# Kernel optimization log

Measured on AMD Instinct MI355X. Metric: run time of the kernel, lower is better.

Reference implementation:

```python
import jax, jax.numpy as jnp
import numpy as np


def _dequantize_and_unpack(packed, scales):
    """packed: [d_out, d_in//2] int8, each byte holds two 4-bit nibbles.
    Returns [d_out, d_in] in scales.dtype, scaled per output row."""
    low = (packed & 15).astype(jnp.int8)
    high = (packed >> 4).astype(jnp.int8)  # arithmetic shift, like torch int8 >> 4
    low = jnp.where(low > 7, low - 16, low)
    high = jnp.where(high > 7, high - 16, high)
    # interleave: even cols = high nibble, odd cols = low nibble
    w = jnp.stack([high, low], axis=-1).reshape(packed.shape[0], -1)
    return w.astype(scales.dtype) * scales


def setup_inputs() -> dict:
    key = jax.random.key(0)
    ks = jax.random.split(key, 7)
    d = 4096
    N = 4096
    x = jax.random.normal(ks[0], (N, d), dtype=jnp.float32)
    fc1_weights_packed = jax.random.randint(ks[1], (2 * d, d // 2), -8, 7, dtype=jnp.int32).astype(jnp.int8)
    fc1_scales = (jax.random.normal(ks[2], (2 * d, 1), dtype=jnp.float32) * 0.02).astype(jnp.float16)
    fc1_bias = jax.random.normal(ks[3], (2 * d,), dtype=jnp.float32)
    fc2_weights_packed = jax.random.randint(ks[4], (d, d), -8, 7, dtype=jnp.int32).astype(jnp.int8)
    fc2_scales = (jax.random.normal(ks[5], (d, 1), dtype=jnp.float32) * 0.02).astype(jnp.float16)
    fc2_bias = jax.random.normal(ks[6], (d,), dtype=jnp.float32)
    return {
        "x": x,
        "fc1_weights_packed": fc1_weights_packed,
        "fc1_scales": fc1_scales,
        "fc1_bias": fc1_bias,
        "fc2_weights_packed": fc2_weights_packed,
        "fc2_scales": fc2_scales,
        "fc2_bias": fc2_bias,
    }


def reference(x, fc1_weights_packed, fc1_scales, fc1_bias,
              fc2_weights_packed, fc2_scales, fc2_bias):
    # fc1: dequantize to [2d, d], linear, relu
    w1 = _dequantize_and_unpack(fc1_weights_packed, fc1_scales).astype(x.dtype)
    h = jax.nn.relu(jnp.dot(x, w1.T) + fc1_bias)
    # fc2: dequantize to [d, 2d], linear
    w2 = _dequantize_and_unpack(fc2_weights_packed, fc2_scales).astype(x.dtype)
    return jnp.dot(h, w2.T) + fc2_bias
```

## Files before the change

kernel.cpp:

```cpp
#include <hip/hip_runtime.h>
#include <hip/hip_fp16.h>
#include <stdint.h>


typedef __attribute__((ext_vector_type(4)))  int i32x4;
typedef __attribute__((ext_vector_type(16))) int i32x16;
typedef __attribute__((ext_vector_type(8))) _Float16 f16x8;

__device__ __forceinline__ void load_lds16(const void* g, void* l) {
    __builtin_amdgcn_global_load_lds(
        (__attribute__((address_space(1))) void*)(void*)g,
        (__attribute__((address_space(3))) void*)(void*)l,
        16, 0, 0);
}

__device__ __forceinline__ float block_max(float m, int tid) {
    __shared__ float red[4];
#pragma unroll
    for (int off = 32; off; off >>= 1)
        m = fmaxf(m, __shfl_down(m, off, 64));
    if ((tid & 63) == 0) red[tid >> 6] = m;
    __syncthreads();
    m = fmaxf(fmaxf(red[0], red[1]), fmaxf(red[2], red[3]));
    __syncthreads();
    return m;
}

__global__ __launch_bounds__(256) void quant_x(
    const float* __restrict__ in, int* __restrict__ out,
    float* __restrict__ rscale, int ncols)
{
    const int tid = threadIdx.x;
    const int row = blockIdx.x;
    const float4* rp = (const float4*)(in + (size_t)row * ncols);
    const int nf4 = ncols / 4;
    float4 v[4];
    float m = 0.f;
#pragma unroll
    for (int k = 0; k < 4; ++k) {
        v[k] = rp[k * 256 + tid];
        m = fmaxf(m, fmaxf(fmaxf(fabsf(v[k].x), fabsf(v[k].y)),
                           fmaxf(fabsf(v[k].z), fabsf(v[k].w))));
    }
    m = block_max(m, tid);
    m = fmaxf(m, 1e-20f);
    const float inv = 127.f / m;
    if (tid == 0) rscale[row] = m / 127.f;
    int* orow = out + (size_t)row * nf4;
#pragma unroll
    for (int k = 0; k < 4; ++k) {
        int q0 = __float2int_rn(v[k].x * inv);
        int q1 = __float2int_rn(v[k].y * inv);
        int q2 = __float2int_rn(v[k].z * inv);
        int q3 = __float2int_rn(v[k].w * inv);
        orow[k * 256 + tid] = (q0 & 0xFF) | ((q1 & 0xFF) << 8) |
                              ((q2 & 0xFF) << 16) | ((q3 & 0xFF) << 24);
    }
}

__global__ __launch_bounds__(256) void quant_h(
    const _Float16* __restrict__ in, int2* __restrict__ out,
    float* __restrict__ rscale, int ncols)
{
    const int tid = threadIdx.x;
    const int row = blockIdx.x;
    const f16x8* rp = (const f16x8*)(in + (size_t)row * ncols);
    const int nv = ncols / 8;
    f16x8 v[4];
    float m = 0.f;
#pragma unroll
    for (int k = 0; k < 4; ++k) {
        v[k] = rp[k * 256 + tid];
#pragma unroll
        for (int e = 0; e < 8; ++e) m = fmaxf(m, (float)v[k][e]);
    }
    m = block_max(m, tid);
    m = fmaxf(m, 1e-20f);
    const float inv = 255.f / m;
    if (tid == 0) rscale[row] = m / 255.f;
    int2* orow = out + (size_t)row * nv;
#pragma unroll
    for (int k = 0; k < 4; ++k) {
        union { int8_t b[8]; int2 w; } u;
#pragma unroll
        for (int e = 0; e < 8; ++e) {
            int q = __float2int_rn((float)v[k][e] * inv);
            q = q < 0 ? 0 : (q > 255 ? 255 : q);
            u.b[e] = (int8_t)(q - 128);
        }
        orow[k * 256 + tid] = u.w;
    }
}

__global__ __launch_bounds__(256) void expand_int4_i8(
    const int4* __restrict__ packed, int2* __restrict__ out,
    int* __restrict__ wsum, int n_i4)
{
    const int tid = threadIdx.x;
    const int row = blockIdx.x;
    const int4* prow = packed + (size_t)row * n_i4;
    int2* orow = out + (size_t)row * n_i4;
    int sum = 0;
    for (int j = tid; j < n_i4; j += 256) {
        int4 p = prow[j];
        int vals[4] = {p.x, p.y, p.z, p.w};
        union { int8_t b[8]; int2 w; } u;
#pragma unroll
        for (int b = 0; b < 4; ++b) {
            int by = (int)(int8_t)(vals[b] & 0xFF);
            int hi = by >> 4;
            int lo = ((by & 15) ^ 8) - 8;
            u.b[2 * b] = (int8_t)hi;
            u.b[2 * b + 1] = (int8_t)lo;
            sum += hi + lo;
        }
        orow[j] = u.w;
    }
    __shared__ int sred[4];
#pragma unroll
    for (int off = 32; off; off >>= 1) sum += __shfl_down(sum, off, 64);
    if ((tid & 63) == 0) sred[tid >> 6] = sum;
    __syncthreads();
    if (tid == 0) wsum[row] = sred[0] + sred[1] + sred[2] + sred[3];
}

template <bool RELU, bool SHIFT, typename OutT>
__global__ __launch_bounds__(512, 2) void gemm_i8_256(
    const int8_t* __restrict__ A, const int8_t* __restrict__ B,
    OutT* __restrict__ C,
    const float* __restrict__ sa,
    const float* __restrict__ s,
    const float* __restrict__ bias,
    const int* __restrict__ wsum,
    int M, int N, int K)
{
    __shared__ alignas(16) char sA[2][256 * 128];
    __shared__ alignas(16) char sB[2][256 * 128];

    const int tid  = threadIdx.x;
    const int lane = tid & 63;
    const int wave = tid >> 6;
    const int wm = wave >> 2;
    const int wn = wave & 3;

    const int nwg = gridDim.x * gridDim.y;
    int bid = blockIdx.y * gridDim.x + blockIdx.x;
    const int cpx = nwg >> 3;
    bid = (bid & 7) * cpx + (bid >> 3);
    const int bm = (bid / gridDim.x) * 256;
    const int bn = (bid % gridDim.x) * 256;

    const int srow = tid >> 3;
    const int scol = ((tid & 7) ^ (srow & 7)) << 4;
    const int8_t* Ag = A + (size_t)(bm + srow) * K + scol;
    const int8_t* Bg = B + (size_t)(bn + srow) * K + scol;
    const size_t rK64 = (size_t)64 * K;
    const int ldst = tid * 16;

    auto stage_a = [&](int buf, int h, int kt) {
        const int8_t* g = Ag + (size_t)h * 128 * K + (size_t)kt * 128;
        char* l = &sA[buf][h * 16384 + ldst];
        load_lds16(g, l);
        load_lds16(g + rK64, l + 8192);
    };
    auto stage_b = [&](int buf, int h, int kt) {
        const int8_t* g = Bg + (size_t)h * 128 * K + (size_t)kt * 128;
        char* l = &sB[buf][h * 16384 + ldst];
        load_lds16(g, l);
        load_lds16(g + rK64, l + 8192);
    };

    const int l31 = lane & 31;
    const int kh  = lane >> 5;
    int coff[4];
#pragma unroll
    for (int ks = 0; ks < 4; ++ks)
        coff[ks] = (((ks * 2 + kh) ^ (l31 & 7)) << 4);
    int abase[4], bbase[2];
#pragma unroll
    for (int i = 0; i < 4; ++i) abase[i] = (wm * 128 + i * 32 + l31) * 128;
#pragma unroll
    for (int j = 0; j < 2; ++j) bbase[j] = (wn * 64 + j * 32 + l31) * 128;

    i32x16 acc[4][2] = {};
    const int NT = K >> 7;

    stage_a(0, 0, 0); stage_a(0, 1, 0);
    stage_b(0, 0, 0); stage_b(0, 1, 0);
    if (NT > 1) { stage_b(1, 0, 1); stage_b(1, 1, 1); }

    for (int t = 0; t < NT; ++t) {
        const char* pA = sA[t & 1];
        const char* pB = sB[t & 1];
        if (t + 1 < NT) asm volatile("s_waitcnt vmcnt(4)" ::: "memory");
        else            asm volatile("s_waitcnt vmcnt(0)" ::: "memory");
        __builtin_amdgcn_s_barrier();
        __builtin_amdgcn_sched_barrier(0);

        i32x4 bf[2][4];
        {
            i32x4 af[4];
#pragma unroll
            for (int j = 0; j < 2; ++j)
#pragma unroll
                for (int ks = 0; ks < 4; ++ks)
                    bf[j][ks] = *(const i32x4*)(pB + bbase[j] + coff[ks]);
#pragma unroll
            for (int ks = 0; ks < 4; ++ks)
                af[ks] = *(const i32x4*)(pA + abase[0] + coff[ks]);
            if (t + 1 < NT) stage_a((t + 1) & 1, 0, t + 1);
            __builtin_amdgcn_s_barrier();
            asm volatile("s_waitcnt lgkmcnt(0)" ::: "memory");
            __builtin_amdgcn_sched_barrier(0);
            __builtin_amdgcn_s_setprio(1);
#pragma unroll
            for (int ks = 0; ks < 4; ++ks) {
                acc[0][0] = __builtin_amdgcn_mfma_i32_32x32x32_i8(
                    af[ks], bf[0][ks], acc[0][0], 0, 0, 0);
                acc[0][1] = __builtin_amdgcn_mfma_i32_32x32x32_i8(
                    af[ks], bf[1][ks], acc[0][1], 0, 0, 0);
            }
            __builtin_amdgcn_s_setprio(0);
            __builtin_amdgcn_s_barrier();
        }
#pragma unroll
        for (int i = 1; i < 4; ++i) {
            i32x4 af[4];
#pragma unroll
            for (int ks = 0; ks < 4; ++ks)
                af[ks] = *(const i32x4*)(pA + abase[i] + coff[ks]);
            if (i == 1)      { if (t + 1 < NT) stage_a((t + 1) & 1, 1, t + 1); }
            else if (i == 2) { if (t + 2 < NT) stage_b(t & 1, 0, t + 2); }
            else             { if (t + 2 < NT) stage_b(t & 1, 1, t + 2); }
            __builtin_amdgcn_s_barrier();
            asm volatile("s_waitcnt lgkmcnt(0)" ::: "memory");
            __builtin_amdgcn_sched_barrier(0);
            __builtin_amdgcn_s_setprio(1);
#pragma unroll
            for (int ks = 0; ks < 4; ++ks) {
                acc[i][0] = __builtin_amdgcn_mfma_i32_32x32x32_i8(
                    af[ks], bf[0][ks], acc[i][0], 0, 0, 0);
                acc[i][1] = __builtin_amdgcn_mfma_i32_32x32x32_i8(
                    af[ks], bf[1][ks], acc[i][1], 0, 0, 0);
            }
            __builtin_amdgcn_s_setprio(0);
            __builtin_amdgcn_s_barrier();
        }
    }

#pragma unroll
    for (int j = 0; j < 2; ++j) {
        const int n  = bn + wn * 64 + j * 32 + l31;
        const float sc = s[n];
        const float bs = bias[n];
        const int shf = SHIFT ? 128 * wsum[n] : 0;
#pragma unroll
        for (int i = 0; i < 4; ++i) {
            const int mb = bm + wm * 128 + i * 32 + 4 * kh;
#pragma unroll
            for (int reg = 0; reg < 16; ++reg) {
                const int m = mb + (reg & 3) + 8 * (reg >> 2);
                float v = (float)(acc[i][j][reg] + shf) * sc * sa[m] + bs;
                if (RELU) v = v > 0.f ? v : 0.f;
                C[(size_t)m * N + n] = (OutT)v;
            }
        }
    }
}

extern "C" void kernel_launch(void* const* d_in, const int* in_sizes, int n_in,
                              void* d_out, int out_size, void* d_ws, size_t ws_size,
                              hipStream_t stream)
{
    const float* x   = (const float*)d_in[0];
    const int4*  w1p = (const int4*)d_in[1];
    const float* s1  = (const float*)d_in[2];
    const float* b1  = (const float*)d_in[3];
    const int4*  w2p = (const int4*)d_in[4];
    const float* s2  = (const float*)d_in[5];
    const float* b2  = (const float*)d_in[6];
    float* out = (float*)d_out;

    const int d    = in_sizes[6];
    const int d2   = in_sizes[3];
    const int Ntok = in_sizes[0] / d;

    char* ws = (char*)d_ws;
    int8_t*   xq = (int8_t*)ws;
    int8_t*   wq = (int8_t*)(ws + (size_t)Ntok * d);
    _Float16* hb = (_Float16*)(ws + (size_t)Ntok * d + (size_t)d2 * d);
    int8_t*   hq = (int8_t*)((char*)hb + (size_t)Ntok * d2 * 2);
    float*    sx = (float*)((char*)hq + (size_t)Ntok * d2);
    float*    sh = sx + Ntok;
    int*      wsum = (int*)(sh + Ntok);

    quant_x<<<Ntok, 256, 0, stream>>>(x, (int*)xq, sx, d);
    expand_int4_i8<<<d2, 256, 0, stream>>>(w1p, (int2*)wq, wsum, d / 8);
    {
        dim3 grid(d2 / 256, Ntok / 256);
        gemm_i8_256<true, false, _Float16><<<grid, 512, 0, stream>>>(
            xq, wq, hb, sx, s1, b1, nullptr, Ntok, d2, d);
    }
    quant_h<<<Ntok, 256, 0, stream>>>(hb, (int2*)hq, sh, d2);
    expand_int4_i8<<<d, 256, 0, stream>>>(w2p, (int2*)wq, wsum, d2 / 8);
    {
        dim3 grid(d / 256, Ntok / 256);
        gemm_i8_256<false, true, float><<<grid, 512, 0, stream>>>(
            hq, wq, out, sh, s2, b2, wsum, Ntok, d, d2);
    }
}
```

Before: 519.9 us.

## Double-buffer A fragments and drop per-row barriers in int8 GEMM main loop

The main loop now keeps two register sets of A fragments, so the next row's LDS reads are issued before the current row's MFMAs. Partial lgkmcnt waits replace full drains, and most of the per-row workgroup barriers are removed. The block-to-tile remap also changes so each XCD owns a contiguous set of column tiles and walks down M. This adds register pressure and relies on the remaining barrier to keep LDS overwrites safe.

```diff
diff --git a/kernel.cpp b/kernel.cpp
--- a/kernel.cpp
+++ b/kernel.cpp
@@ -143,12 +143,14 @@
     const int wm = wave >> 2;
     const int wn = wave & 3;
 
-    const int nwg = gridDim.x * gridDim.y;
     int bid = blockIdx.y * gridDim.x + blockIdx.x;
-    const int cpx = nwg >> 3;
-    bid = (bid & 7) * cpx + (bid >> 3);
-    const int bm = (bid / gridDim.x) * 256;
-    const int bn = (bid % gridDim.x) * 256;
+    const int xcd = bid & 7;
+    const int idx = bid >> 3;
+    const int cpx = gridDim.x >> 3;
+    const int bx = xcd * cpx + idx / gridDim.y;
+    const int by = idx % gridDim.y;
+    const int bm = by * 256;
+    const int bn = bx * 256;
 
     const int srow = tid >> 3;
     const int scol = ((tid & 7) ^ (srow & 7)) << 4;
@@ -189,6 +191,19 @@
     stage_b(0, 0, 0); stage_b(0, 1, 0);
     if (NT > 1) { stage_b(1, 0, 1); stage_b(1, 1, 1); }
 
+#define MFMA_ROW(ri, AF)                                                   \
+    do {                                                                   \
+        __builtin_amdgcn_s_setprio(1);                                     \
+        _Pragma("unroll")                                                  \
+        for (int ks = 0; ks < 4; ++ks) {                                   \
+            acc[ri][0] = __builtin_amdgcn_mfma_i32_32x32x32_i8(            \
+                AF[ks], bf[0][ks], acc[ri][0], 0, 0, 0);                   \
+            acc[ri][1] = __builtin_amdgcn_mfma_i32_32x32x32_i8(            \
+                AF[ks], bf[1][ks], acc[ri][1], 0, 0, 0);                   \
+        }                                                                  \
+        __builtin_amdgcn_s_setprio(0);                                     \
+    } while (0)
+
     for (int t = 0; t < NT; ++t) {
         const char* pA = sA[t & 1];
         const char* pB = sB[t & 1];
@@ -197,56 +212,51 @@
         __builtin_amdgcn_s_barrier();
         __builtin_amdgcn_sched_barrier(0);
 
-        i32x4 bf[2][4];
-        {
-            i32x4 af[4];
-#pragma unroll
-            for (int j = 0; j < 2; ++j)
-#pragma unroll
-                for (int ks = 0; ks < 4; ++ks)
-                    bf[j][ks] = *(const i32x4*)(pB + bbase[j] + coff[ks]);
+        i32x4 bf[2][4], afA[4], afB[4];
+#pragma unroll
+        for (int j = 0; j < 2; ++j)
 #pragma unroll
             for (int ks = 0; ks < 4; ++ks)
-                af[ks] = *(const i32x4*)(pA + abase[0] + coff[ks]);
-            if (t + 1 < NT) stage_a((t + 1) & 1, 0, t + 1);
-            __builtin_amdgcn_s_barrier();
-            asm volatile("s_waitcnt lgkmcnt(0)" ::: "memory");
-            __builtin_amdgcn_sched_barrier(0);
-            __builtin_amdgcn_s_setprio(1);
-#pragma unroll
-            for (int ks = 0; ks < 4; ++ks) {
-                acc[0][0] = __builtin_amdgcn_mfma_i32_32x32x32_i8(
-                    af[ks], bf[0][ks], acc[0][0], 0, 0, 0);
-                acc[0][1] = __builtin_amdgcn_mfma_i32_32x32x32_i8(
-                    af[ks], bf[1][ks], acc[0][1], 0, 0, 0);
-            }
-            __builtin_amdgcn_s_setprio(0);
-            __builtin_amdgcn_s_barrier();
-        }
-#pragma unroll
-        for (int i = 1; i < 4; ++i) {
-            i32x4 af[4];
-#pragma unroll
-            for (int ks = 0; ks < 4; ++ks)
-                af[ks] = *(const i32x4*)(pA + abase[i] + coff[ks]);
-            if (i == 1)      { if (t + 1 < NT) stage_a((t + 1) & 1, 1, t + 1); }
-            else if (i == 2) { if (t + 2 < NT) stage_b(t & 1, 0, t + 2); }
-            else             { if (t + 2 < NT) stage_b(t & 1, 1, t + 2); }
-            __builtin_amdgcn_s_barrier();
-            asm volatile("s_waitcnt lgkmcnt(0)" ::: "memory");
-            __builtin_amdgcn_sched_barrier(0);
-            __builtin_amdgcn_s_setprio(1);
-#pragma unroll
-            for (int ks = 0; ks < 4; ++ks) {
-                acc[i][0] = __builtin_amdgcn_mfma_i32_32x32x32_i8(
-                    af[ks], bf[0][ks], acc[i][0], 0, 0, 0);
-                acc[i][1] = __builtin_amdgcn_mfma_i32_32x32x32_i8(
-                    af[ks], bf[1][ks], acc[i][1], 0, 0, 0);
-            }
-            __builtin_amdgcn_s_setprio(0);
-            __builtin_amdgcn_s_barrier();
-        }
-    }
+                bf[j][ks] = *(const i32x4*)(pB + bbase[j] + coff[ks]);
+#pragma unroll
+        for (int ks = 0; ks < 4; ++ks)
+            afA[ks] = *(const i32x4*)(pA + abase[0] + coff[ks]);
+#pragma unroll
+        for (int ks = 0; ks < 4; ++ks)
+            afB[ks] = *(const i32x4*)(pA + abase[1] + coff[ks]);
+        if (t + 1 < NT) stage_a((t + 1) & 1, 0, t + 1);
+        __builtin_amdgcn_sched_barrier(0);
+        asm volatile("s_waitcnt lgkmcnt(4)" ::: "memory");
+        __builtin_amdgcn_sched_barrier(0);
+        MFMA_ROW(0, afA);
+
+#pragma unroll
+        for (int ks = 0; ks < 4; ++ks)
+            afA[ks] = *(const i32x4*)(pA + abase[2] + coff[ks]);
+        if (t + 1 < NT) stage_a((t + 1) & 1, 1, t + 1);
+        __builtin_amdgcn_sched_barrier(0);
+        asm volatile("s_waitcnt lgkmcnt(4)" ::: "memory");
+        __builtin_amdgcn_sched_barrier(0);
+        MFMA_ROW(1, afB);
+
+        __builtin_amdgcn_s_barrier();
+        __builtin_amdgcn_sched_barrier(0);
+#pragma unroll
+        for (int ks = 0; ks < 4; ++ks)
+            afB[ks] = *(const i32x4*)(pA + abase[3] + coff[ks]);
+        if (t + 2 < NT) stage_b(t & 1, 0, t + 2);
+        __builtin_amdgcn_sched_barrier(0);
+        asm volatile("s_waitcnt lgkmcnt(4)" ::: "memory");
+        __builtin_amdgcn_sched_barrier(0);
+        MFMA_ROW(2, afA);
+
+        if (t + 2 < NT) stage_b(t & 1, 1, t + 2);
+        __builtin_amdgcn_sched_barrier(0);
+        asm volatile("s_waitcnt lgkmcnt(0)" ::: "memory");
+        __builtin_amdgcn_sched_barrier(0);
+        MFMA_ROW(3, afB);
+    }
+#undef MFMA_ROW
 
 #pragma unroll
     for (int j = 0; j < 2; ++j) {
```

New measurement: 502.7 us. -3.3%, faster.

## Pre-swizzle quantized activations into MFMA fragment layout and load A directly to registers

Applied to the files above, without the earlier changes.

The quantizers now write int8 activations in a blocked layout of 32-row by 16-byte chunks, matching the MFMA A-operand fragment order. The GEMM loads A fragments straight from global memory into registers, skipping LDS for A. Only B is still staged through LDS, now via register loads and ds_writes instead of global_load_lds, with a reworked software pipeline that double-buffers A fragments across k-steps. This cuts LDS traffic and halves LDS use, at the cost of more register pressure and exposed global latency on A.

```diff
diff --git a/kernel.cpp b/kernel.cpp
--- a/kernel.cpp
+++ b/kernel.cpp
@@ -6,13 +6,6 @@
 typedef __attribute__((ext_vector_type(4)))  int i32x4;
 typedef __attribute__((ext_vector_type(16))) int i32x16;
 typedef __attribute__((ext_vector_type(8))) _Float16 f16x8;
-
-__device__ __forceinline__ void load_lds16(const void* g, void* l) {
-    __builtin_amdgcn_global_load_lds(
-        (__attribute__((address_space(1))) void*)(void*)g,
-        (__attribute__((address_space(3))) void*)(void*)l,
-        16, 0, 0);
-}
 
 __device__ __forceinline__ float block_max(float m, int tid) {
     __shared__ float red[4];
@@ -27,18 +20,17 @@
 }
 
 __global__ __launch_bounds__(256) void quant_x(
-    const float* __restrict__ in, int* __restrict__ out,
+    const float* __restrict__ in, int4* __restrict__ out,
     float* __restrict__ rscale, int ncols)
 {
     const int tid = threadIdx.x;
     const int row = blockIdx.x;
-    const float4* rp = (const float4*)(in + (size_t)row * ncols);
-    const int nf4 = ncols / 4;
+    const float4* r4 = (const float4*)(in + (size_t)row * ncols);
     float4 v[4];
     float m = 0.f;
 #pragma unroll
     for (int k = 0; k < 4; ++k) {
-        v[k] = rp[k * 256 + tid];
+        v[k] = r4[tid * 4 + k];
         m = fmaxf(m, fmaxf(fmaxf(fabsf(v[k].x), fabsf(v[k].y)),
                            fmaxf(fabsf(v[k].z), fabsf(v[k].w))));
     }
@@ -46,49 +38,52 @@
     m = fmaxf(m, 1e-20f);
     const float inv = 127.f / m;
     if (tid == 0) rscale[row] = m / 127.f;
-    int* orow = out + (size_t)row * nf4;
+    union { int8_t b[16]; int4 w; } u;
 #pragma unroll
     for (int k = 0; k < 4; ++k) {
-        int q0 = __float2int_rn(v[k].x * inv);
-        int q1 = __float2int_rn(v[k].y * inv);
-        int q2 = __float2int_rn(v[k].z * inv);
-        int q3 = __float2int_rn(v[k].w * inv);
-        orow[k * 256 + tid] = (q0 & 0xFF) | ((q1 & 0xFF) << 8) |
-                              ((q2 & 0xFF) << 16) | ((q3 & 0xFF) << 24);
-    }
+        u.b[4 * k + 0] = (int8_t)__float2int_rn(v[k].x * inv);
+        u.b[4 * k + 1] = (int8_t)__float2int_rn(v[k].y * inv);
+        u.b[4 * k + 2] = (int8_t)__float2int_rn(v[k].z * inv);
+        u.b[4 * k + 3] = (int8_t)__float2int_rn(v[k].w * inv);
+    }
+    out[((size_t)(row >> 5) * (ncols >> 4) + tid) * 32 + (row & 31)] = u.w;
 }
 
 __global__ __launch_bounds__(256) void quant_h(
-    const _Float16* __restrict__ in, int2* __restrict__ out,
+    const _Float16* __restrict__ in, int4* __restrict__ out,
     float* __restrict__ rscale, int ncols)
 {
     const int tid = threadIdx.x;
     const int row = blockIdx.x;
     const f16x8* rp = (const f16x8*)(in + (size_t)row * ncols);
-    const int nv = ncols / 8;
-    f16x8 v[4];
+    f16x8 v[2][2];
     float m = 0.f;
 #pragma unroll
-    for (int k = 0; k < 4; ++k) {
-        v[k] = rp[k * 256 + tid];
-#pragma unroll
-        for (int e = 0; e < 8; ++e) m = fmaxf(m, (float)v[k][e]);
+    for (int c = 0; c < 2; ++c) {
+        const int kc = tid + c * 256;
+        v[c][0] = rp[2 * kc];
+        v[c][1] = rp[2 * kc + 1];
+#pragma unroll
+        for (int e = 0; e < 8; ++e)
+            m = fmaxf(m, fmaxf((float)v[c][0][e], (float)v[c][1][e]));
     }
     m = block_max(m, tid);
     m = fmaxf(m, 1e-20f);
     const float inv = 255.f / m;
     if (tid == 0) rscale[row] = m / 255.f;
-    int2* orow = out + (size_t)row * nv;
-#pragma unroll
-    for (int k = 0; k < 4; ++k) {
-        union { int8_t b[8]; int2 w; } u;
-#pragma unroll
-        for (int e = 0; e < 8; ++e) {
-            int q = __float2int_rn((float)v[k][e] * inv);
-            q = q < 0 ? 0 : (q > 255 ? 255 : q);
-            u.b[e] = (int8_t)(q - 128);
-        }
-        orow[k * 256 + tid] = u.w;
+#pragma unroll
+    for (int c = 0; c < 2; ++c) {
+        const int kc = tid + c * 256;
+        union { int8_t b[16]; int4 w; } u;
+#pragma unroll
+        for (int h = 0; h < 2; ++h)
+#pragma unroll
+            for (int e = 0; e < 8; ++e) {
+                int q = __float2int_rn((float)v[c][h][e] * inv);
+                q = q < 0 ? 0 : (q > 255 ? 255 : q);
+                u.b[8 * h + e] = (int8_t)(q - 128);
+            }
+        out[((size_t)(row >> 5) * (ncols >> 4) + kc) * 32 + (row & 31)] = u.w;
     }
 }
 
@@ -125,16 +120,14 @@
 }
 
 template <bool RELU, bool SHIFT, typename OutT>
-__global__ __launch_bounds__(512, 2) void gemm_i8_256(
-    const int8_t* __restrict__ A, const int8_t* __restrict__ B,
+__global__ __launch_bounds__(512, 2) void gemm_i8_ad(
+    const int8_t* __restrict__ Ablk,
+    const int8_t* __restrict__ B,
     OutT* __restrict__ C,
-    const float* __restrict__ sa,
-    const float* __restrict__ s,
-    const float* __restrict__ bias,
-    const int* __restrict__ wsum,
+    const float* __restrict__ sa, const float* __restrict__ s,
+    const float* __restrict__ bias, const int* __restrict__ wsum,
     int M, int N, int K)
 {
-    __shared__ alignas(16) char sA[2][256 * 128];
     __shared__ alignas(16) char sB[2][256 * 128];
 
     const int tid  = threadIdx.x;
@@ -143,32 +136,20 @@
     const int wm = wave >> 2;
     const int wn = wave & 3;
 
-    const int nwg = gridDim.x * gridDim.y;
     int bid = blockIdx.y * gridDim.x + blockIdx.x;
-    const int cpx = nwg >> 3;
+    const int cpx = (gridDim.x * gridDim.y) >> 3;
     bid = (bid & 7) * cpx + (bid >> 3);
     const int bm = (bid / gridDim.x) * 256;
     const int bn = (bid % gridDim.x) * 256;
 
-    const int srow = tid >> 3;
-    const int scol = ((tid & 7) ^ (srow & 7)) << 4;
-    const int8_t* Ag = A + (size_t)(bm + srow) * K + scol;
-    const int8_t* Bg = B + (size_t)(bn + srow) * K + scol;
+    const int br = tid >> 3;
+    const int bc = tid & 7;
+    const int8_t* Bg2 = B + (size_t)(bn + br) * K + bc * 16;
     const size_t rK64 = (size_t)64 * K;
-    const int ldst = tid * 16;
-
-    auto stage_a = [&](int buf, int h, int kt) {
-        const int8_t* g = Ag + (size_t)h * 128 * K + (size_t)kt * 128;
-        char* l = &sA[buf][h * 16384 + ldst];
-        load_lds16(g, l);
-        load_lds16(g + rK64, l + 8192);
-    };
-    auto stage_b = [&](int buf, int h, int kt) {
-        const int8_t* g = Bg + (size_t)h * 128 * K + (size_t)kt * 128;
-        char* l = &sB[buf][h * 16384 + ldst];
-        load_lds16(g, l);
-        load_lds16(g + rK64, l + 8192);
-    };
+    int bw[4];
+#pragma unroll
+    for (int h = 0; h < 4; ++h)
+        bw[h] = (br + 64 * h) * 128 + ((bc ^ (br & 7)) << 4);
 
     const int l31 = lane & 31;
     const int kh  = lane >> 5;
@@ -176,77 +157,101 @@
 #pragma unroll
     for (int ks = 0; ks < 4; ++ks)
         coff[ks] = (((ks * 2 + kh) ^ (l31 & 7)) << 4);
-    int abase[4], bbase[2];
-#pragma unroll
-    for (int i = 0; i < 4; ++i) abase[i] = (wm * 128 + i * 32 + l31) * 128;
+    int bbase[2];
 #pragma unroll
     for (int j = 0; j < 2; ++j) bbase[j] = (wn * 64 + j * 32 + l31) * 128;
 
+    const int KC = K >> 4;
+    const char* apb[4];
+#pragma unroll
+    for (int i = 0; i < 4; ++i)
+        apb[i] = (const char*)Ablk +
+                 ((size_t)((bm >> 5) + wm * 4 + i) * KC + (size_t)kh) * 512 +
+                 (size_t)(l31 * 16);
+    size_t ga = 0;
+
+    i32x4 afX[4], afY[4], bfX[2], bfY[2], bsr[4];
     i32x16 acc[4][2] = {};
     const int NT = K >> 7;
 
-    stage_a(0, 0, 0); stage_a(0, 1, 0);
-    stage_b(0, 0, 0); stage_b(0, 1, 0);
-    if (NT > 1) { stage_b(1, 0, 1); stage_b(1, 1, 1); }
+#define SB0() __builtin_amdgcn_sched_barrier(0)
+#define AFISSUE(AF)                                                         \
+    do { _Pragma("unroll")                                                  \
+        for (int i_ = 0; i_ < 4; ++i_)                                      \
+            AF[i_] = *(const i32x4*)(apb[i_] + ga);                         \
+        ga += 1024; } while (0)
+#define BFREAD(BF, KS)                                                      \
+    do { BF[0] = *(const i32x4*)(pB + bbase[0] + coff[KS]);                 \
+         BF[1] = *(const i32x4*)(pB + bbase[1] + coff[KS]); } while (0)
+#define MFMA8(AF, BF)                                                       \
+    do { __builtin_amdgcn_s_setprio(1);                                     \
+        _Pragma("unroll")                                                   \
+        for (int i_ = 0; i_ < 4; ++i_) {                                    \
+            acc[i_][0] = __builtin_amdgcn_mfma_i32_32x32x32_i8(             \
+                AF[i_], BF[0], acc[i_][0], 0, 0, 0);                        \
+            acc[i_][1] = __builtin_amdgcn_mfma_i32_32x32x32_i8(             \
+                AF[i_], BF[1], acc[i_][1], 0, 0, 0);                        \
+        }                                                                   \
+        __builtin_amdgcn_s_setprio(0); } while (0)
+
+    AFISSUE(afX);
+    AFISSUE(afY);
+    {
+#pragma unroll
+        for (int h = 0; h < 4; ++h)
+            bsr[h] = *(const i32x4*)(Bg2 + (size_t)h * rK64);
+#pragma unroll
+        for (int h = 0; h < 4; ++h)
+            *(i32x4*)(sB[0] + bw[h]) = bsr[h];
+    }
+    asm volatile("s_waitcnt lgkmcnt(0)" ::: "memory");
+    SB0();
+    __builtin_amdgcn_s_barrier();
+    SB0();
 
     for (int t = 0; t < NT; ++t) {
-        const char* pA = sA[t & 1];
         const char* pB = sB[t & 1];
-        if (t + 1 < NT) asm volatile("s_waitcnt vmcnt(4)" ::: "memory");
-        else            asm volatile("s_waitcnt vmcnt(0)" ::: "memory");
-        __builtin_amdgcn_s_barrier();
-        __builtin_amdgcn_sched_barrier(0);
-
-        i32x4 bf[2][4];
-        {
-            i32x4 af[4];
-#pragma unroll
-            for (int j = 0; j < 2; ++j)
-#pragma unroll
-                for (int ks = 0; ks < 4; ++ks)
-                    bf[j][ks] = *(const i32x4*)(pB + bbase[j] + coff[ks]);
-#pragma unroll
-            for (int ks = 0; ks < 4; ++ks)
-                af[ks] = *(const i32x4*)(pA + abase[0] + coff[ks]);
-            if (t + 1 < NT) stage_a((t + 1) & 1, 0, t + 1);
-            __builtin_amdgcn_s_barrier();
+        char* pW = sB[(t + 1) & 1];
+        const bool pf = (t + 1 < NT);
+
+        BFREAD(bfX, 0);
+        BFREAD(bfY, 1);
+        if (pf) {
+            const int8_t* bsrc = Bg2 + (size_t)(t + 1) * 128;
+#pragma unroll
+            for (int h = 0; h < 4; ++h)
+                bsr[h] = *(const i32x4*)(bsrc + (size_t)h * rK64);
+        }
+        SB0();
+        MFMA8(afX, bfX);
+        AFISSUE(afX);
+        SB0();
+        BFREAD(bfX, 2);
+        SB0();
+        MFMA8(afY, bfY);
+        AFISSUE(afY);
+        SB0();
+        BFREAD(bfY, 3);
+        SB0();
+        MFMA8(afX, bfX);
+        if (pf) AFISSUE(afX);
+        SB0();
+        MFMA8(afY, bfY);
+        if (pf) {
+            AFISSUE(afY);
+#pragma unroll
+            for (int h = 0; h < 4; ++h)
+                *(i32x4*)(pW + bw[h]) = bsr[h];
             asm volatile("s_waitcnt lgkmcnt(0)" ::: "memory");
-            __builtin_amdgcn_sched_barrier(0);
-            __builtin_amdgcn_s_setprio(1);
-#pragma unroll
-            for (int ks = 0; ks < 4; ++ks) {
-                acc[0][0] = __builtin_amdgcn_mfma_i32_32x32x32_i8(
-                    af[ks], bf[0][ks], acc[0][0], 0, 0, 0);
-                acc[0][1] = __builtin_amdgcn_mfma_i32_32x32x32_i8(
-                    af[ks], bf[1][ks], acc[0][1], 0, 0, 0);
-            }
-            __builtin_amdgcn_s_setprio(0);
+            SB0();
             __builtin_amdgcn_s_barrier();
         }
-#pragma unroll
-        for (int i = 1; i < 4; ++i) {
-            i32x4 af[4];
-#pragma unroll
-            for (int ks = 0; ks < 4; ++ks)
-                af[ks] = *(const i32x4*)(pA + abase[i] + coff[ks]);
-            if (i == 1)      { if (t + 1 < NT) stage_a((t + 1) & 1, 1, t + 1); }
-            else if (i == 2) { if (t + 2 < NT) stage_b(t & 1, 0, t + 2); }
-            else             { if (t + 2 < NT) stage_b(t & 1, 1, t + 2); }
-            __builtin_amdgcn_s_barrier();
-            asm volatile("s_waitcnt lgkmcnt(0)" ::: "memory");
-            __builtin_amdgcn_sched_barrier(0);
-            __builtin_amdgcn_s_setprio(1);
-#pragma unroll
-            for (int ks = 0; ks < 4; ++ks) {
-                acc[i][0] = __builtin_amdgcn_mfma_i32_32x32x32_i8(
-                    af[ks], bf[0][ks], acc[i][0], 0, 0, 0);
-                acc[i][1] = __builtin_amdgcn_mfma_i32_32x32x32_i8(
-                    af[ks], bf[1][ks], acc[i][1], 0, 0, 0);
-            }
-            __builtin_amdgcn_s_setprio(0);
-            __builtin_amdgcn_s_barrier();
-        }
-    }
+        SB0();
+    }
+#undef SB0
+#undef AFISSUE
+#undef BFREAD
+#undef MFMA8
 
 #pragma unroll
     for (int j = 0; j < 2; ++j) {
@@ -294,18 +299,18 @@
     float*    sh = sx + Ntok;
     int*      wsum = (int*)(sh + Ntok);
 
-    quant_x<<<Ntok, 256, 0, stream>>>(x, (int*)xq, sx, d);
+    quant_x<<<Ntok, 256, 0, stream>>>(x, (int4*)xq, sx, d);
     expand_int4_i8<<<d2, 256, 0, stream>>>(w1p, (int2*)wq, wsum, d / 8);
     {
         dim3 grid(d2 / 256, Ntok / 256);
-        gemm_i8_256<true, false, _Float16><<<grid, 512, 0, stream>>>(
+        gemm_i8_ad<true, false, _Float16><<<grid, 512, 0, stream>>>(
             xq, wq, hb, sx, s1, b1, nullptr, Ntok, d2, d);
     }
-    quant_h<<<Ntok, 256, 0, stream>>>(hb, (int2*)hq, sh, d2);
+    quant_h<<<Ntok, 256, 0, stream>>>(hb, (int4*)hq, sh, d2);
     expand_int4_i8<<<d, 256, 0, stream>>>(w2p, (int2*)wq, wsum, d2 / 8);
     {
         dim3 grid(d / 256, Ntok / 256);
-        gemm_i8_256<false, true, float><<<grid, 512, 0, stream>>>(
+        gemm_i8_ad<false, true, float><<<grid, 512, 0, stream>>>(
             hq, wq, out, sh, s2, b2, wsum, Ntok, d, d2);
     }
 }
```

Measured after the change: 579.7 us. 1.12x slower.
